# Kernel tuning notes

Hardware: AMD Instinct MI355X
Metric: run time of the kernel (lower is better)

## Reference

```python
import jax, jax.numpy as jnp
import numpy as np

EPS = 1e-5


def _conv1x1(x, w, b=None):
    # x: [B,C,H,W], w: [O,C]
    y = jnp.einsum('bchw,oc->bohw', x, w)
    if b is not None:
        y = y + b[None, :, None, None]
    return y


def _bn(x, g, b, m, v):
    inv = g / jnp.sqrt(v + EPS)
    return x * inv[None, :, None, None] + (b - m * inv)[None, :, None, None]


def setup_inputs() -> dict:
    key = jax.random.key(0)
    ks = jax.random.split(key, 24)
    B, Cin, H, W = 4, 512, 64, 64
    Ci = Cin // 8  # 64
    s = 0.05
    d = {}
    d['x'] = jax.random.normal(ks[0], (B, Cin, H, W), jnp.float32)
    # conv_p1 (BasicConv2d: conv no-bias + BN)
    d['wp1'] = jax.random.normal(ks[1], (Ci, Cin), jnp.float32) * s
    d['gp1'] = jnp.ones((Ci,), jnp.float32)
    d['bp1'] = jnp.zeros((Ci,), jnp.float32)
    d['mp1'] = jax.random.normal(ks[2], (Ci,), jnp.float32) * 0.1
    d['vp1'] = jax.random.uniform(ks[3], (Ci,), jnp.float32, 0.5, 1.5)
    # conv_c1
    d['wc1'] = jax.random.normal(ks[4], (Ci, Cin), jnp.float32) * s
    d['gc1'] = jnp.ones((Ci,), jnp.float32)
    d['bc1'] = jnp.zeros((Ci,), jnp.float32)
    d['mc1'] = jax.random.normal(ks[5], (Ci,), jnp.float32) * 0.1
    d['vc1'] = jax.random.uniform(ks[6], (Ci,), jnp.float32, 0.5, 1.5)
    # PAM 1x1 convs (with bias)
    d['wb'] = jax.random.normal(ks[7], (Ci, Ci), jnp.float32) * s
    d['bb'] = jnp.zeros((Ci,), jnp.float32)
    d['wc2'] = jax.random.normal(ks[8], (Ci, Ci), jnp.float32) * s
    d['bc2'] = jnp.zeros((Ci,), jnp.float32)
    d['wd'] = jax.random.normal(ks[9], (Ci, Ci), jnp.float32) * s
    d['bd'] = jnp.zeros((Ci,), jnp.float32)
    d['alpha'] = jnp.array([0.5], jnp.float32)  # nonzero so attention path is exercised
    d['beta'] = jnp.array([0.5], jnp.float32)
    # out conv
    d['wo'] = jax.random.normal(ks[10], (Cin, Ci), jnp.float32) * s
    d['go'] = jnp.ones((Cin,), jnp.float32)
    d['bo'] = jnp.zeros((Cin,), jnp.float32)
    d['mo'] = jax.random.normal(ks[11], (Cin,), jnp.float32) * 0.1
    d['vo'] = jax.random.uniform(ks[12], (Cin,), jnp.float32, 0.5, 1.5)
    return d


def reference(x, wp1, gp1, bp1, mp1, vp1, wc1, gc1, bc1, mc1, vc1,
              wb, bb, wc2, bc2, wd, bd, alpha, beta, wo, go, bo, mo, vo):
    B, Cin, H, W = x.shape
    HW = H * W

    # --- position branch ---
    fp = _bn(_conv1x1(x, wp1), gp1, bp1, mp1, vp1)          # [B,Ci,H,W]
    Ci = fp.shape[1]
    fb = _conv1x1(fp, wb, bb).reshape(B, Ci, HW)             # query  [B,Ci,HW]
    fc = _conv1x1(fp, wc2, bc2).reshape(B, Ci, HW)           # key    [B,Ci,HW]
    fd = _conv1x1(fp, wd, bd).reshape(B, Ci, HW)             # value  [B,Ci,HW]
    attn_s = jax.nn.softmax(jnp.einsum('bcq,bck->bqk', fb, fc), axis=-1)  # [B,HW,HW]
    feat_ep = jnp.einsum('bck,bqk->bcq', fd, attn_s).reshape(B, Ci, H, W)
    feat_p = alpha[0] * feat_ep + fp

    # --- channel branch ---
    fcb = _bn(_conv1x1(x, wc1), gc1, bc1, mc1, vc1)          # [B,Ci,H,W]
    fa = fcb.reshape(B, Ci, HW)
    attn_c = jnp.einsum('bcn,bdn->bcd', fa, fa)              # [B,Ci,Ci]
    attn_c = jnp.max(attn_c, axis=-1, keepdims=True) - attn_c
    attn_c = jax.nn.softmax(attn_c, axis=-1)
    feat_ec = jnp.einsum('bcd,bdn->bcn', attn_c, fa).reshape(B, Ci, H, W)
    feat_c = beta[0] * feat_ec + fcb

    # --- fuse + out ---
    fusion = feat_p + feat_c
    out = _bn(_conv1x1(fusion, wo), go, bo, mo, vo)          # [B,Cin,H,W]
    return out
```

## Files before the change

kernel.cpp:

```cpp
#include <hip/hip_runtime.h>
#include <hip/hip_bf16.h>

typedef __hip_bfloat16 bf16;
typedef unsigned short u16;
typedef __attribute__((ext_vector_type(8))) short short8;
typedef __attribute__((ext_vector_type(4))) float f32x4;

#define HW 4096
#define NB (64*HW)

__device__ __forceinline__ f32x4 MFMA16(short8 a, short8 b, f32x4 c){
  return __builtin_amdgcn_mfma_f32_16x16x32_bf16(a, b, c, 0, 0, 0);
}

__device__ __forceinline__ short f2bf(float f){
  bf16 h = __float2bfloat16(f);
  return *(short*)&h;
}

__global__ __launch_bounds__(256) void k_const(float* __restrict__ out, float v, int n){
  int i = blockIdx.x*256 + threadIdx.x;
  if (i < n) out[i] = v;
}

__global__ __launch_bounds__(512) void k_prep(
    const float* __restrict__ gp, const float* __restrict__ bp,
    const float* __restrict__ mp, const float* __restrict__ vp,
    const float* __restrict__ gc, const float* __restrict__ bc,
    const float* __restrict__ mc, const float* __restrict__ vc,
    const float* __restrict__ go, const float* __restrict__ bo,
    const float* __restrict__ mo, const float* __restrict__ vo,
    float* __restrict__ bn){
  int t = threadIdx.x;
  if (t < 64){
    float iv = gp[t] * rsqrtf(vp[t] + 1e-5f);
    bn[t] = iv; bn[64+t] = bp[t] - mp[t]*iv;
    float ic = gc[t] * rsqrtf(vc[t] + 1e-5f);
    bn[128+t] = ic; bn[192+t] = bc[t] - mc[t]*ic;
  }
  float io = go[t] * rsqrtf(vo[t] + 1e-5f);
  bn[256+t] = io; bn[768+t] = bo[t] - mo[t]*io;
}

__global__ __launch_bounds__(256) void k_conv_in(
    const float* __restrict__ x, const float* __restrict__ wp1, const float* __restrict__ wc1,
    const float* __restrict__ bn, float* __restrict__ fp, float* __restrict__ fcb){
  __shared__ __align__(16) float Wl[512][16];
  const int t = threadIdx.x;
  const int cg = blockIdx.y, b = blockIdx.z;
  const bool isP = cg < 4;
  const int c0 = (cg & 3) * 16;
  const float* w = isP ? wp1 : wc1;
  const float* inv  = isP ? bn       : bn + 128;
  const float* bias = isP ? bn + 64  : bn + 192;
  float* outp = isP ? fp : fcb;
  for (int i = t; i < 8192; i += 256){
    int c = i & 15, k = i >> 4;
    Wl[k][c] = w[(size_t)(c0 + c)*512 + k];
  }
  __syncthreads();
  const int p = blockIdx.x*256 + t;
  const float* xb = x + (size_t)b*512*HW + p;
  float acc[16];
  #pragma unroll
  for (int i = 0; i < 16; i++) acc[i] = 0.f;
  for (int k = 0; k < 512; k++){
    float xv = xb[(size_t)k*HW];
    float4 w0 = *(const float4*)&Wl[k][0];
    float4 w1 = *(const float4*)&Wl[k][4];
    float4 w2 = *(const float4*)&Wl[k][8];
    float4 w3 = *(const float4*)&Wl[k][12];
    acc[0]=fmaf(w0.x,xv,acc[0]); acc[1]=fmaf(w0.y,xv,acc[1]); acc[2]=fmaf(w0.z,xv,acc[2]); acc[3]=fmaf(w0.w,xv,acc[3]);
    acc[4]=fmaf(w1.x,xv,acc[4]); acc[5]=fmaf(w1.y,xv,acc[5]); acc[6]=fmaf(w1.z,xv,acc[6]); acc[7]=fmaf(w1.w,xv,acc[7]);
    acc[8]=fmaf(w2.x,xv,acc[8]); acc[9]=fmaf(w2.y,xv,acc[9]); acc[10]=fmaf(w2.z,xv,acc[10]); acc[11]=fmaf(w2.w,xv,acc[11]);
    acc[12]=fmaf(w3.x,xv,acc[12]); acc[13]=fmaf(w3.y,xv,acc[13]); acc[14]=fmaf(w3.z,xv,acc[14]); acc[15]=fmaf(w3.w,xv,acc[15]);
  }
  const size_t base = (size_t)b*NB + p;
  #pragma unroll
  for (int i = 0; i < 16; i++){
    int c = c0 + i;
    outp[base + (size_t)c*HW] = fmaf(acc[i], inv[c], bias[c]);
  }
}

__global__ __launch_bounds__(256) void k_qkv(
    const float* __restrict__ fp,
    const float* __restrict__ wb,  const float* __restrict__ bbv,
    const float* __restrict__ wc2, const float* __restrict__ bc2,
    const float* __restrict__ wd,  const float* __restrict__ bd,
    bf16* __restrict__ fB, bf16* __restrict__ fC, bf16* __restrict__ fD){
  __shared__ __align__(16) float Wl[64][16];
  __shared__ float Bl[16];
  const int t = threadIdx.x;
  const int mg = blockIdx.y, mat = mg >> 2, c0 = (mg & 3)*16, b = blockIdx.z;
  const float* w    = (mat == 0) ? wb  : (mat == 1 ? wc2 : wd);
  const float* bias = (mat == 0) ? bbv : (mat == 1 ? bc2 : bd);
  bf16* outp        = (mat == 0) ? fB  : (mat == 1 ? fC  : fD);
  for (int i = t; i < 1024; i += 256){
    int c = i & 15, k = i >> 4;
    Wl[k][c] = w[(size_t)(c0 + c)*64 + k];
  }
  if (t < 16) Bl[t] = bias[c0 + t];
  __syncthreads();
  const int p = blockIdx.x*512 + t*2;
  const float* in = fp + (size_t)b*NB + p;
  float2 acc[16];
  #pragma unroll
  for (int i = 0; i < 16; i++){ acc[i].x = 0.f; acc[i].y = 0.f; }
  for (int k = 0; k < 64; k++){
    float2 xv = *(const float2*)(in + (size_t)k*HW);
    float4 w0 = *(const float4*)&Wl[k][0];
    float4 w1 = *(const float4*)&Wl[k][4];
    float4 w2 = *(const float4*)&Wl[k][8];
    float4 w3 = *(const float4*)&Wl[k][12];
    float wv[16] = {w0.x,w0.y,w0.z,w0.w, w1.x,w1.y,w1.z,w1.w,
                    w2.x,w2.y,w2.z,w2.w, w3.x,w3.y,w3.z,w3.w};
    #pragma unroll
    for (int i = 0; i < 16; i++){
      acc[i].x = fmaf(wv[i], xv.x, acc[i].x);
      acc[i].y = fmaf(wv[i], xv.y, acc[i].y);
    }
  }
  if (mat < 2){
    bf16* ob = outp + (size_t)b*NB;
    #pragma unroll
    for (int i = 0; i < 16; i += 2){
      __hip_bfloat162 h0 = __float22bfloat162_rn(
          make_float2(acc[i].x + Bl[i], acc[i+1].x + Bl[i+1]));
      __hip_bfloat162 h1 = __float22bfloat162_rn(
          make_float2(acc[i].y + Bl[i], acc[i+1].y + Bl[i+1]));
      *(__hip_bfloat162*)&ob[(size_t)p*64 + c0 + i]     = h0;
      *(__hip_bfloat162*)&ob[(size_t)(p+1)*64 + c0 + i] = h1;
    }
  } else {
    const size_t base = (size_t)b*NB + p;
    #pragma unroll
    for (int i = 0; i < 16; i++){
      float bl = Bl[i];
      __hip_bfloat162 o2 = __float22bfloat162_rn(make_float2(acc[i].x + bl, acc[i].y + bl));
      *(__hip_bfloat162*)&outp[base + (size_t)(c0 + i)*HW] = o2;
    }
  }
}

__global__ __launch_bounds__(256) void k_chan_attn(
    const float* __restrict__ fcb, float* __restrict__ attn){
  __shared__ __align__(16) float rowc[4096];
  __shared__ float red[256];
  __shared__ float Srow[64];
  const int c = blockIdx.x, b = blockIdx.y, t = threadIdx.x;
  const float* fa = fcb + (size_t)b*NB;
  #pragma unroll
  for (int i = 0; i < 4; i++){
    int n = i*1024 + t*4;
    *(float4*)&rowc[n] = *(const float4*)&fa[(size_t)c*HW + n];
  }
  __syncthreads();
  const int d = t >> 2, part = t & 3;
  const float* frow = fa + (size_t)d*HW + part*1024;
  const float* rc = rowc + part*1024;
  float s = 0.f;
  for (int i = 0; i < 1024; i += 4){
    float4 xv = *(const float4*)&frow[i];
    float4 rv = *(const float4*)&rc[i];
    s += xv.x*rv.x + xv.y*rv.y + xv.z*rv.z + xv.w*rv.w;
  }
  red[t] = s;
  __syncthreads();
  if (part == 0) Srow[d] = red[t] + red[t+1] + red[t+2] + red[t+3];
  __syncthreads();
  if (t < 64){
    float z = -Srow[t];
    float m = z;
    #pragma unroll
    for (int off = 32; off; off >>= 1) m = fmaxf(m, __shfl_xor(m, off));
    float e = __expf(fminf(z - m, 0.f));
    float ss = e;
    #pragma unroll
    for (int off = 32; off; off >>= 1) ss += __shfl_xor(ss, off);
    attn[(size_t)b*4096 + (size_t)c*64 + t] = e / ss;
  }
}

__global__ __attribute__((amdgpu_flat_work_group_size(512, 512), amdgpu_waves_per_eu(2, 2)))
void k_pos_attn(
    const u16* __restrict__ fBt, const u16* __restrict__ fCt, const u16* __restrict__ fDv,
    const float* __restrict__ fpl, const float* __restrict__ alphap,
    float* __restrict__ fus){
  __shared__ __align__(16) u16 Kt[2][128*72];
  __shared__ __align__(16) u16 Vt[2][64*136];

  const int t = threadIdx.x;
  const int b = blockIdx.y, q0 = blockIdx.x*64;
  const int wv = t>>6;
  const int g  = wv>>2;
  const int wg = wv&3;
  const int lane = t&63, quad = lane>>4, lr = lane&15;
  const int tg = t & 255;
  const u16* Fb = fBt + (size_t)b*NB;
  const u16* Fc = fCt + (size_t)b*NB;
  const u16* Fd = fDv + (size_t)b*NB;

  const size_t qoff = (size_t)(q0 + wg*16 + lr)*64;
  short8 a0 = *(const short8*)&Fb[qoff + quad*8];
  short8 a1 = *(const short8*)&Fb[qoff + 32 + quad*8];

  const int krbase = ((lr>>2)<<3) + (lr&3);

  float m = -3.0e38f, l = 0.f;
  f32x4 accO[4];
  #pragma unroll
  for (int cs = 0; cs < 4; cs++) accO[cs] = (f32x4){0.f,0.f,0.f,0.f};

  const int skk = tg>>1, sch = (tg&1)*32;
  const int svc = tg>>2, svk = (tg&3)*32;
  const u16* Ksrc = Fc + (size_t)(g*2048 + skk)*64 + sch;
  const u16* Vsrc = Fd + (size_t)svc*HW + g*2048 + svk;

  uint4 kr[4], vr[4];
  #pragma unroll
  for (int i = 0; i < 4; i++){
    kr[i] = ((const uint4*)Ksrc)[i];
    vr[i] = ((const uint4*)Vsrc)[i];
  }

  for (int tile = 0; tile < 16; ++tile){
    __syncthreads();
    {
      u16* kd = &Kt[g][skk*72 + sch];
      u16* vd = &Vt[g][svc*136 + svk];
      #pragma unroll
      for (int i = 0; i < 4; i++) ((uint4*)kd)[i] = kr[i];
      #pragma unroll
      for (int i = 0; i < 4; i++) ((uint4*)vd)[i] = vr[i];
    }
    __syncthreads();

    if (tile < 15){
      const u16* ks2 = Ksrc + (size_t)(tile+1)*128*64;
      const u16* vs2 = Vsrc + (tile+1)*128;
      #pragma unroll
      for (int i = 0; i < 4; i++){
        kr[i] = ((const uint4*)ks2)[i];
        vr[i] = ((const uint4*)vs2)[i];
      }
    }

    f32x4 s[8];
    #pragma unroll
    for (int ks = 0; ks < 8; ks++){
      const int krow = krbase + ((ks>>1)<<5) + ((ks&1)<<2);
      short8 k0 = *(short8*)&Kt[g][krow*72 + quad*8];
      short8 k1 = *(short8*)&Kt[g][krow*72 + 32 + quad*8];
      f32x4 acc = {0.f,0.f,0.f,0.f};
      acc = MFMA16(k0, a0, acc);
      acc = MFMA16(k1, a1, acc);
      s[ks] = acc;
    }

    float t4[8];
    #pragma unroll
    for (int ks = 0; ks < 8; ks++)
      t4[ks] = fmaxf(fmaxf(s[ks][0], s[ks][1]), fmaxf(s[ks][2], s[ks][3]));
    float mx = fmaxf(fmaxf(fmaxf(t4[0],t4[1]), fmaxf(t4[2],t4[3])),
                     fmaxf(fmaxf(t4[4],t4[5]), fmaxf(t4[6],t4[7])));
    mx = fmaxf(mx, __shfl_xor(mx, 16));
    mx = fmaxf(mx, __shfl_xor(mx, 32));
    const float mn = fmaxf(m, mx);
    const float al = __expf(m - mn);
    m = mn;

    short8 pf0, pf1, pf2, pf3;
    float rs = 0.f;
    #pragma unroll
    for (int ks = 0; ks < 8; ks++){
      float e0 = __expf(s[ks][0] - m);
      float e1 = __expf(s[ks][1] - m);
      float e2 = __expf(s[ks][2] - m);
      float e3 = __expf(s[ks][3] - m);
      rs += (e0 + e1) + (e2 + e3);
      const int o = (ks&1)*4;
      short b0 = f2bf(e0), b1 = f2bf(e1), b2 = f2bf(e2), b3 = f2bf(e3);
      if ((ks>>1) == 0){ pf0[o]=b0; pf0[o+1]=b1; pf0[o+2]=b2; pf0[o+3]=b3; }
      else if ((ks>>1) == 1){ pf1[o]=b0; pf1[o+1]=b1; pf1[o+2]=b2; pf1[o+3]=b3; }
      else if ((ks>>1) == 2){ pf2[o]=b0; pf2[o+1]=b1; pf2[o+2]=b2; pf2[o+3]=b3; }
      else            { pf3[o]=b0; pf3[o+1]=b1; pf3[o+2]=b2; pf3[o+3]=b3; }
    }
    rs += __shfl_xor(rs, 16);
    rs += __shfl_xor(rs, 32);
    l = l*al + rs;
    #pragma unroll
    for (int cs = 0; cs < 4; cs++) accO[cs] *= al;

    #pragma unroll
    for (int cs = 0; cs < 4; cs++){
      short8 vf0 = *(short8*)&Vt[g][(cs*16+lr)*136 +  0 + quad*8];
      short8 vf1 = *(short8*)&Vt[g][(cs*16+lr)*136 + 32 + quad*8];
      short8 vf2 = *(short8*)&Vt[g][(cs*16+lr)*136 + 64 + quad*8];
      short8 vf3 = *(short8*)&Vt[g][(cs*16+lr)*136 + 96 + quad*8];
      accO[cs] = MFMA16(vf0, pf0, accO[cs]);
      accO[cs] = MFMA16(vf1, pf1, accO[cs]);
      accO[cs] = MFMA16(vf2, pf2, accO[cs]);
      accO[cs] = MFMA16(vf3, pf3, accO[cs]);
    }
  }

  __syncthreads();
  float* Ol = (float*)&Kt[0][0];
  float* Ml = Ol + 64*69;
  float* Ll = Ml + 64;
  if (g == 1){
    const int row = wg*16 + lr;
    #pragma unroll
    for (int cs = 0; cs < 4; cs++){
      #pragma unroll
      for (int r = 0; r < 4; r++)
        Ol[row*69 + cs*16 + quad*4 + r] = accO[cs][r];
    }
    if (quad == 0){ Ml[row] = m; Ll[row] = l; }
  }
  __syncthreads();
  if (g == 0){
    const float alp = alphap[0];
    const int row = wg*16 + lr;
    const float m1 = Ml[row], l1 = Ll[row];
    const float mt = fmaxf(m, m1);
    const float e0 = __expf(m - mt), e1 = __expf(m1 - mt);
    const float lt = fmaxf(l*e0 + l1*e1, 1e-20f);
    const float sc = alp / lt;
    #pragma unroll
    for (int cs = 0; cs < 4; cs++){
      #pragma unroll
      for (int r = 0; r < 4; r++){
        int idx = row*69 + cs*16 + quad*4 + r;
        Ol[idx] = (accO[cs][r]*e0 + Ol[idx]*e1) * sc;
      }
    }
  }
  __syncthreads();

  {
    const int c = t >> 3, qs = (t & 7) * 8;
    const float* Fp = fpl + (size_t)b*NB + (size_t)c*HW + q0 + qs;
    float* Fo = fus + (size_t)b*NB + (size_t)c*HW + q0 + qs;
    float v[8];
    #pragma unroll
    for (int j = 0; j < 8; j++) v[j] = Ol[(qs+j)*69 + c] + Fp[j];
    *(float4*)&Fo[0] = make_float4(v[0],v[1],v[2],v[3]);
    *(float4*)&Fo[4] = make_float4(v[4],v[5],v[6],v[7]);
  }
}

__global__ __launch_bounds__(256) void k_chan_apply(
    const float* __restrict__ fcb, const float* __restrict__ attn,
    const float* __restrict__ betap, float* __restrict__ fus){
  __shared__ __align__(16) float Ar2[64][8];
  const int t = threadIdx.x;
  const int c0 = blockIdx.y*8, b = blockIdx.z;
  for (int i = t; i < 512; i += 256){
    int d = i >> 3, ci = i & 7;
    Ar2[d][ci] = attn[(size_t)b*4096 + (size_t)(c0 + ci)*64 + d];
  }
  __syncthreads();
  const int p = blockIdx.x*256 + t;
  const float* fa = fcb + (size_t)b*NB;
  float acc[8] = {0.f,0.f,0.f,0.f,0.f,0.f,0.f,0.f};
  for (int d = 0; d < 64; d++){
    float v = fa[(size_t)d*HW + p];
    float4 A0 = *(const float4*)&Ar2[d][0];
    float4 A1 = *(const float4*)&Ar2[d][4];
    acc[0]=fmaf(A0.x,v,acc[0]); acc[1]=fmaf(A0.y,v,acc[1]); acc[2]=fmaf(A0.z,v,acc[2]); acc[3]=fmaf(A0.w,v,acc[3]);
    acc[4]=fmaf(A1.x,v,acc[4]); acc[5]=fmaf(A1.y,v,acc[5]); acc[6]=fmaf(A1.z,v,acc[6]); acc[7]=fmaf(A1.w,v,acc[7]);
  }
  const float be = betap[0];
  #pragma unroll
  for (int i = 0; i < 8; i++){
    size_t idx = (size_t)b*NB + (size_t)(c0 + i)*HW + p;
    fus[idx] += fmaf(be, acc[i], fa[(size_t)(c0 + i)*HW + p]);
  }
}

__global__ __launch_bounds__(256) void k_conv_out(
    const float* __restrict__ fus, const float* __restrict__ wo,
    const float* __restrict__ bn, float* __restrict__ out){
  __shared__ __align__(16) float Wl[64][16];
  const int t = threadIdx.x;
  const int o0 = blockIdx.y*16, b = blockIdx.z;
  for (int i = t; i < 1024; i += 256){
    int o = i & 15, c = i >> 4;
    Wl[c][o] = wo[(size_t)(o0 + o)*64 + c];
  }
  __syncthreads();
  const int p = blockIdx.x*512 + t*2;
  const float* fu = fus + (size_t)b*NB + p;
  float2 acc[16];
  #pragma unroll
  for (int i = 0; i < 16; i++){ acc[i].x = 0.f; acc[i].y = 0.f; }
  for (int c = 0; c < 64; c++){
    float2 xv = *(const float2*)(fu + (size_t)c*HW);
    float4 w0 = *(const float4*)&Wl[c][0];
    float4 w1 = *(const float4*)&Wl[c][4];
    float4 w2 = *(const float4*)&Wl[c][8];
    float4 w3 = *(const float4*)&Wl[c][12];
    float wv[16] = {w0.x,w0.y,w0.z,w0.w, w1.x,w1.y,w1.z,w1.w,
                    w2.x,w2.y,w2.z,w2.w, w3.x,w3.y,w3.z,w3.w};
    #pragma unroll
    for (int i = 0; i < 16; i++){
      acc[i].x = fmaf(wv[i], xv.x, acc[i].x);
      acc[i].y = fmaf(wv[i], xv.y, acc[i].y);
    }
  }
  #pragma unroll
  for (int i = 0; i < 16; i++){
    int o = o0 + i;
    float iv = bn[256+o], bs = bn[768+o];
    float* op = &out[(size_t)b*512*HW + (size_t)o*HW + p];
    op[0] = fmaf(acc[i].x, iv, bs);
    op[1] = fmaf(acc[i].y, iv, bs);
  }
}

extern "C" void kernel_launch(void* const* d_in, const int* in_sizes, int n_in,
                              void* d_out, int out_size, void* d_ws, size_t ws_size,
                              hipStream_t stream){
  static const int dictSz[24] = {8388608,32768,64,64,64,64,32768,64,64,64,64,
                                 4096,64,4096,64,4096,64,1,1,32768,512,512,512,512};
  bool dictOk = (n_in == 24);
  if (dictOk){
    for (int i = 0; i < 24; i++) if (in_sizes[i] != dictSz[i]) dictOk = false;
  }
  bool wsOk = (ws_size >= (size_t)(19u << 20));
  float* out = (float*)d_out;
  if (!dictOk){ k_const<<<(out_size+255)/256, 256, 0, stream>>>(out, 32.f, out_size); return; }
  if (!wsOk)  { k_const<<<(out_size+255)/256, 256, 0, stream>>>(out, 48.f, out_size); return; }

  const float* x    = (const float*)d_in[0];
  const float* wp1  = (const float*)d_in[1];
  const float* gp1  = (const float*)d_in[2];  const float* bp1 = (const float*)d_in[3];
  const float* mp1  = (const float*)d_in[4];  const float* vp1 = (const float*)d_in[5];
  const float* wc1  = (const float*)d_in[6];
  const float* gc1  = (const float*)d_in[7];  const float* bc1 = (const float*)d_in[8];
  const float* mc1  = (const float*)d_in[9];  const float* vc1 = (const float*)d_in[10];
  const float* wb   = (const float*)d_in[11]; const float* bb  = (const float*)d_in[12];
  const float* wc2  = (const float*)d_in[13]; const float* bc2 = (const float*)d_in[14];
  const float* wd   = (const float*)d_in[15]; const float* bd  = (const float*)d_in[16];
  const float* alp  = (const float*)d_in[17]; const float* bet = (const float*)d_in[18];
  const float* wo   = (const float*)d_in[19];
  const float* go   = (const float*)d_in[20]; const float* bo  = (const float*)d_in[21];
  const float* mo   = (const float*)d_in[22]; const float* vo  = (const float*)d_in[23];

  char* w8 = (char*)d_ws;
  float* fp    = (float*)(w8);
  float* fcb   = (float*)(w8 + (4u<<20));
  float* fus   = (float*)(w8 + (8u<<20));
  bf16*  fB    = (bf16*) (w8 + (12u<<20));
  bf16*  fC    = (bf16*) (w8 + (14u<<20));
  bf16*  fD    = (bf16*) (w8 + (16u<<20));
  float* attnc = (float*)(w8 + (18u<<20));
  float* bn    = (float*)(w8 + (18u<<20) + 65536);

  k_prep<<<1, 512, 0, stream>>>(gp1,bp1,mp1,vp1, gc1,bc1,mc1,vc1, go,bo,mo,vo, bn);
  k_conv_in<<<dim3(16,8,4), 256, 0, stream>>>(x, wp1, wc1, bn, fp, fcb);
  k_qkv<<<dim3(8,12,4), 256, 0, stream>>>(fp, wb,bb, wc2,bc2, wd,bd, fB, fC, fD);
  k_chan_attn<<<dim3(64,4), 256, 0, stream>>>(fcb, attnc);
  k_pos_attn<<<dim3(64,4), 512, 0, stream>>>((const u16*)fB, (const u16*)fC, (const u16*)fD,
                                             fp, alp, fus);
  k_chan_apply<<<dim3(16,8,4), 256, 0, stream>>>(fcb, attnc, bet, fus);
  k_conv_out<<<dim3(8,32,4), 256, 0, stream>>>(fus, wo, bn, out);
}
```

Baseline: 326.8 us.

## Halve position-attention block size and load K/V tiles directly into LDS

Measured after the change: 316.0 us. -3.3%, faster.

```diff
diff --git a/kernel.cpp b/kernel.cpp
--- a/kernel.cpp
+++ b/kernel.cpp
@@ -182,7 +182,7 @@
   }
 }
 
-__global__ __attribute__((amdgpu_flat_work_group_size(512, 512), amdgpu_waves_per_eu(2, 2)))
+__global__ __attribute__((amdgpu_flat_work_group_size(256, 256), amdgpu_waves_per_eu(2, 2)))
 void k_pos_attn(
     const u16* __restrict__ fBt, const u16* __restrict__ fCt, const u16* __restrict__ fDv,
     const float* __restrict__ fpl, const float* __restrict__ alphap,
@@ -191,12 +191,12 @@
   __shared__ __align__(16) u16 Vt[2][64*136];
 
   const int t = threadIdx.x;
-  const int b = blockIdx.y, q0 = blockIdx.x*64;
+  const int b = blockIdx.y, q0 = blockIdx.x*32;
   const int wv = t>>6;
-  const int g  = wv>>2;
-  const int wg = wv&3;
+  const int g  = wv>>1;
+  const int wg = wv&1;
   const int lane = t&63, quad = lane>>4, lr = lane&15;
-  const int tg = t & 255;
+  const int tg = t & 127;
   const u16* Fb = fBt + (size_t)b*NB;
   const u16* Fc = fCt + (size_t)b*NB;
   const u16* Fd = fDv + (size_t)b*NB;
@@ -212,39 +212,22 @@
   #pragma unroll
   for (int cs = 0; cs < 4; cs++) accO[cs] = (f32x4){0.f,0.f,0.f,0.f};
 
-  const int skk = tg>>1, sch = (tg&1)*32;
-  const int svc = tg>>2, svk = (tg&3)*32;
-  const u16* Ksrc = Fc + (size_t)(g*2048 + skk)*64 + sch;
-  const u16* Vsrc = Fd + (size_t)svc*HW + g*2048 + svk;
-
-  uint4 kr[4], vr[4];
-  #pragma unroll
-  for (int i = 0; i < 4; i++){
-    kr[i] = ((const uint4*)Ksrc)[i];
-    vr[i] = ((const uint4*)Vsrc)[i];
-  }
+  const u16* Ksrc = Fc + (size_t)(g*2048 + tg)*64;
+  const u16* Vsrc = Fd + (size_t)(tg>>1)*HW + g*2048 + (tg&1)*64;
+  u16* Kdst = &Kt[g][tg*72];
+  u16* Vdst = &Vt[g][(tg>>1)*136 + (tg&1)*64];
 
   for (int tile = 0; tile < 16; ++tile){
     __syncthreads();
     {
-      u16* kd = &Kt[g][skk*72 + sch];
-      u16* vd = &Vt[g][svc*136 + svk];
+      const uint4* ks = (const uint4*)(Ksrc + (size_t)tile*128*64);
+      const uint4* vs = (const uint4*)(Vsrc + tile*128);
       #pragma unroll
-      for (int i = 0; i < 4; i++) ((uint4*)kd)[i] = kr[i];
+      for (int i = 0; i < 8; i++) ((uint4*)Kdst)[i] = ks[i];
       #pragma unroll
-      for (int i = 0; i < 4; i++) ((uint4*)vd)[i] = vr[i];
+      for (int i = 0; i < 8; i++) ((uint4*)Vdst)[i] = vs[i];
     }
     __syncthreads();
-
-    if (tile < 15){
-      const u16* ks2 = Ksrc + (size_t)(tile+1)*128*64;
-      const u16* vs2 = Vsrc + (tile+1)*128;
-      #pragma unroll
-      for (int i = 0; i < 4; i++){
-        kr[i] = ((const uint4*)ks2)[i];
-        vr[i] = ((const uint4*)vs2)[i];
-      }
-    }
 
     f32x4 s[8];
     #pragma unroll
@@ -307,8 +290,8 @@
 
   __syncthreads();
   float* Ol = (float*)&Kt[0][0];
-  float* Ml = Ol + 64*69;
-  float* Ll = Ml + 64;
+  float* Ml = Ol + 32*69;
+  float* Ll = Ml + 32;
   if (g == 1){
     const int row = wg*16 + lr;
     #pragma unroll
@@ -340,7 +323,7 @@
   __syncthreads();
 
   {
-    const int c = t >> 3, qs = (t & 7) * 8;
+    const int c = t >> 2, qs = (t & 3) * 8;
     const float* Fp = fpl + (size_t)b*NB + (size_t)c*HW + q0 + qs;
     float* Fo = fus + (size_t)b*NB + (size_t)c*HW + q0 + qs;
     float v[8];
@@ -463,8 +446,8 @@
   k_conv_in<<<dim3(16,8,4), 256, 0, stream>>>(x, wp1, wc1, bn, fp, fcb);
   k_qkv<<<dim3(8,12,4), 256, 0, stream>>>(fp, wb,bb, wc2,bc2, wd,bd, fB, fC, fD);
   k_chan_attn<<<dim3(64,4), 256, 0, stream>>>(fcb, attnc);
-  k_pos_attn<<<dim3(64,4), 512, 0, stream>>>((const u16*)fB, (const u16*)fC, (const u16*)fD,
-                                             fp, alp, fus);
+  k_pos_attn<<<dim3(128,4), 256, 0, stream>>>((const u16*)fB, (const u16*)fC, (const u16*)fD,
+                                              fp, alp, fus);
   k_chan_apply<<<dim3(16,8,4), 256, 0, stream>>>(fcb, attnc, bet, fus);
   k_conv_out<<<dim3(8,32,4), 256, 0, stream>>>(fus, wo, bn, out);
 }
```
